# Kernel tuning notes

Hardware: AMD Instinct MI355X
Metric: run time of the kernel (lower is better)

Reference implementation:

```python
import jax, jax.numpy as jnp
import numpy as np

DEST = 64          # args['output_size']
NET = 256          # network_size = input_size - 3*dest_size
INPUT = NET + 3 * DEST  # 448
B, N = 4, 2048


def setup_inputs() -> dict:
    key = jax.random.key(0)
    ks = jax.random.split(key, 9)
    node_feature = jax.random.normal(ks[0], (B, N, INPUT), jnp.float32)
    adj_forward = jax.random.uniform(ks[1], (B, N, N), jnp.float32)
    adj_backward = jax.random.uniform(ks[2], (B, N, N), jnp.float32)
    s = 1.0 / np.sqrt(2 * DEST)
    Wf = jax.random.normal(ks[3], (2 * DEST, DEST), jnp.float32) * s
    bf = jnp.zeros((DEST,), jnp.float32)
    Wb = jax.random.normal(ks[4], (2 * DEST, DEST), jnp.float32) * s
    bb = jnp.zeros((DEST,), jnp.float32)
    W_emb = jax.random.normal(ks[5], (NET, 2 * DEST), jnp.float32) / np.sqrt(NET)
    b_emb = jnp.zeros((2 * DEST,), jnp.float32)
    return {"node_feature": node_feature, "adj_forward": adj_forward,
            "adj_backward": adj_backward, "Wf": Wf, "bf": bf,
            "Wb": Wb, "bb": bb, "W_emb": W_emb, "b_emb": b_emb}


def _gcn(x, adj, W, b):
    # GCN layer: aggregate neighbors then project. x: [B,N,2d], adj: [B,N,N]
    h = jnp.einsum('bmn,bnf->bmf', adj, x)  # message passing
    return h @ W + b                         # [B,N,d]


def reference(node_feature, adj_forward, adj_backward, Wf, bf, Wb, bb, W_emb, b_emb):
    dyn = node_feature[:, :, :DEST]                 # [B,N,d]
    struct = node_feature[:, :, DEST:3 * DEST]      # [B,N,2d]
    stat = node_feature[:, :, 3 * DEST:]            # [B,N,NET]
    fwd_code = dyn * _gcn(struct, adj_forward, Wf, bf)
    bwd_code = dyn * _gcn(struct, adj_backward, Wb, bb)
    emb = jnp.concatenate((fwd_code, bwd_code), axis=2)  # [B,N,2d]
    gate = jax.nn.sigmoid(stat @ W_emb + b_emb)           # [B,N,2d]
    return emb * gate
```

## Files before the change

kernel.cpp:

```cpp
#include <hip/hip_runtime.h>
#include <hip/hip_bf16.h>
#include <math.h>

#define BB    4
#define NNODE 2048
#define DST   64
#define NETW  256
#define INPT  448

typedef float f32x4 __attribute__((ext_vector_type(4)));
typedef short s16x8 __attribute__((ext_vector_type(8)));

#define MFMA(a, b, c) __builtin_amdgcn_mfma_f32_16x16x32_bf16((a), (b), (c), 0, 0, 0)

__device__ __align__(16) unsigned short g_WcatT[128 * 128];
__device__ __align__(16) unsigned short g_WembT[128 * 256];
__device__ __align__(16) unsigned short g_Ut[BB * 128 * NNODE];
__device__ __align__(16) float          g_G2[BB * NNODE * 128];

__device__ __forceinline__ unsigned bf16pk(float a, float b) {
    unsigned ua = __builtin_bit_cast(unsigned, a);
    unsigned ub = __builtin_bit_cast(unsigned, b);
    ua += 0x7fffu + ((ua >> 16) & 1u);
    ub += 0x7fffu + ((ub >> 16) & 1u);
    return (ua >> 16) | (ub & 0xffff0000u);
}
__device__ __forceinline__ unsigned short bf16b(float a) {
    unsigned ua = __builtin_bit_cast(unsigned, a);
    ua += 0x7fffu + ((ua >> 16) & 1u);
    return (unsigned short)(ua >> 16);
}
__device__ __forceinline__ s16x8 pack8(float4 x, float4 y) {
    union { unsigned u[4]; s16x8 s; } r;
    r.u[0] = bf16pk(x.x, x.y);
    r.u[1] = bf16pk(x.z, x.w);
    r.u[2] = bf16pk(y.x, y.y);
    r.u[3] = bf16pk(y.z, y.w);
    return r.s;
}

__global__ void k_weights(const float* __restrict__ Wf, const float* __restrict__ Wb,
                          const float* __restrict__ We) {
    int t = blockIdx.x * blockDim.x + threadIdx.x;
    int stride = gridDim.x * blockDim.x;
    for (int i = t; i < 128 * 128; i += stride) {
        int j = i >> 7, f = i & 127;
        float v = (j < 64) ? Wf[f * 64 + j] : Wb[f * 64 + (j - 64)];
        g_WcatT[i] = bf16b(v);
    }
    for (int i = t; i < 128 * 256; i += stride) {
        int c = i >> 8, k = i & 255;
        g_WembT[i] = bf16b(We[k * 128 + c]);
    }
}

__global__ __launch_bounds__(256) void k_prep(const float* __restrict__ nfeat,
                                              const float* __restrict__ bemb) {
    int w  = threadIdx.x >> 6;
    int l  = threadIdx.x & 63;
    int lr = l & 15, lc = l >> 4;
    int bid = blockIdx.x;

    if (bid < 512) {
        int b = bid >> 7;
        int nbase = (bid & 127) * 16;
        f32x4 acc[2] = {};
        #pragma unroll
        for (int kg = 0; kg < 4; ++kg) {
            s16x8 a0 = *(const s16x8*)&g_WcatT[((2 * w + 0) * 16 + lr) * 128 + kg * 32 + lc * 8];
            s16x8 a1 = *(const s16x8*)&g_WcatT[((2 * w + 1) * 16 + lr) * 128 + kg * 32 + lc * 8];
            const float* p = nfeat + (size_t)(b * NNODE + nbase + lr) * INPT + DST + kg * 32 + lc * 8;
            float4 x0 = *(const float4*)p;
            float4 x1 = *(const float4*)(p + 4);
            s16x8 bfr = pack8(x0, x1);
            acc[0] = MFMA(a0, bfr, acc[0]);
            acc[1] = MFMA(a1, bfr, acc[1]);
        }
        #pragma unroll
        for (int ja = 0; ja < 2; ++ja)
            #pragma unroll
            for (int r = 0; r < 4; ++r) {
                int j = (2 * w + ja) * 16 + lc * 4 + r;
                g_Ut[(size_t)(b * 128 + j) * NNODE + nbase + lr] = bf16b(acc[ja][r]);
            }
    } else {
        int bid2 = bid - 512;
        int b = bid2 >> 7;
        int mbase = (bid2 & 127) * 16;
        f32x4 acc[2] = {};
        #pragma unroll
        for (int kg = 0; kg < 8; ++kg) {
            const float* p = nfeat + (size_t)(b * NNODE + mbase + lr) * INPT + 3 * DST + kg * 32 + lc * 8;
            float4 x0 = *(const float4*)p;
            float4 x1 = *(const float4*)(p + 4);
            s16x8 a = pack8(x0, x1);
            #pragma unroll
            for (int ca = 0; ca < 2; ++ca) {
                int nf = 2 * w + ca;
                s16x8 bfr = *(const s16x8*)&g_WembT[(nf * 16 + lr) * 256 + kg * 32 + lc * 8];
                acc[ca] = MFMA(a, bfr, acc[ca]);
            }
        }
        #pragma unroll
        for (int ca = 0; ca < 2; ++ca) {
            int c = (2 * w + ca) * 16 + lr;
            float be = bemb[c];
            #pragma unroll
            for (int r = 0; r < 4; ++r) {
                int mm = mbase + lc * 4 + r;
                float v = acc[ca][r] + be;
                float g = 1.0f / (1.0f + expf(-v));
                g_G2[(size_t)(b * NNODE + mm) * 128 + c] =
                    g * nfeat[(size_t)(b * NNODE + mm) * INPT + (c & 63)];
            }
        }
    }
}

#define KW 8
__global__ __launch_bounds__(512) void k_main(const float* __restrict__ adjf,
                                              const float* __restrict__ adjb,
                                              const float* __restrict__ biasf,
                                              const float* __restrict__ biasb,
                                              float* __restrict__ out) {
    int bid  = blockIdx.x;
    int tile = bid & 127;
    int dir  = (bid >> 7) & 1;
    int b    = bid >> 8;
    int w  = threadIdx.x >> 6;
    int l  = threadIdx.x & 63;
    int lr = l & 15, lc = l >> 4;

    const float* adj  = dir ? adjb : adjf;
    const float* bias = dir ? biasb : biasf;
    int m0 = tile * 16;
    int k0 = w * 256;
    const float* arow = adj + (size_t)(b * NNODE + m0 + lr) * NNODE + k0 + lc * 8;
    const unsigned short* ut = g_Ut + (size_t)(b * 128 + dir * 64) * NNODE + k0;

    f32x4 acc[4] = {};
    #pragma unroll
    for (int ki = 0; ki < 8; ++ki) {
        const float4* pa = (const float4*)(arow + ki * 32);
        float4 x0 = pa[0];
        float4 x1 = pa[1];
        s16x8 a = pack8(x0, x1);
        #pragma unroll
        for (int nf = 0; nf < 4; ++nf) {
            s16x8 bfr = *(const s16x8*)&ut[(nf * 16 + lr) * NNODE + ki * 32 + lc * 8];
            acc[nf] = MFMA(a, bfr, acc[nf]);
        }
    }

    __shared__ float lds[KW][16][64];
    #pragma unroll
    for (int nf = 0; nf < 4; ++nf)
        #pragma unroll
        for (int r = 0; r < 4; ++r)
            lds[w][nf * 4 + r][l] = acc[nf][r];
    __syncthreads();

    if (w < 4) {
        #pragma unroll
        for (int r = 0; r < 4; ++r) {
            float s = 0.f;
            #pragma unroll
            for (int wp = 0; wp < KW; ++wp)
                s += lds[wp][w * 4 + r][l];
            int col = w * 16 + lr;
            int m   = m0 + lc * 4 + r;
            size_t o = (size_t)(b * NNODE + m) * 128 + dir * 64 + col;
            out[o] = (s + bias[col]) * g_G2[o];
        }
    }
}

extern "C" void kernel_launch(void* const* d_in, const int* in_sizes, int n_in,
                              void* d_out, int out_size, void* d_ws, size_t ws_size,
                              hipStream_t stream) {
    (void)in_sizes; (void)n_in; (void)d_ws; (void)ws_size; (void)out_size;
    const float* nfeat = (const float*)d_in[0];
    const float* adjf  = (const float*)d_in[1];
    const float* adjb  = (const float*)d_in[2];
    const float* Wf    = (const float*)d_in[3];
    const float* bf    = (const float*)d_in[4];
    const float* Wb    = (const float*)d_in[5];
    const float* bb    = (const float*)d_in[6];
    const float* We    = (const float*)d_in[7];
    const float* bemb  = (const float*)d_in[8];
    float* out = (float*)d_out;

    hipLaunchKernelGGL(k_weights, dim3(64),   dim3(256), 0, stream, Wf, Wb, We);
    hipLaunchKernelGGL(k_prep,    dim3(1024), dim3(256), 0, stream, nfeat, bemb);
    hipLaunchKernelGGL(k_main,    dim3(1024), dim3(512), 0, stream, adjf, adjb, bf, bb, out);
}
```

Measured before the change: 224.1 us.

## Pre-swizzle MFMA fragments, stage adjacency through LDS with coalesced loads and prefetch

```diff
diff --git a/kernel.cpp b/kernel.cpp
--- a/kernel.cpp
+++ b/kernel.cpp
@@ -2,174 +2,240 @@
 #include <hip/hip_bf16.h>
 #include <math.h>
 
-#define BB    4
-#define NNODE 2048
-#define DST   64
-#define NETW  256
-#define INPT  448
+#define BB   4
+#define NN   2048
+#define INPT 448
 
 typedef float f32x4 __attribute__((ext_vector_type(4)));
 typedef short s16x8 __attribute__((ext_vector_type(8)));
-
-#define MFMA(a, b, c) __builtin_amdgcn_mfma_f32_16x16x32_bf16((a), (b), (c), 0, 0, 0)
-
-__device__ __align__(16) unsigned short g_WcatT[128 * 128];
-__device__ __align__(16) unsigned short g_WembT[128 * 256];
-__device__ __align__(16) unsigned short g_Ut[BB * 128 * NNODE];
-__device__ __align__(16) float          g_G2[BB * NNODE * 128];
-
-__device__ __forceinline__ unsigned bf16pk(float a, float b) {
-    unsigned ua = __builtin_bit_cast(unsigned, a);
-    unsigned ub = __builtin_bit_cast(unsigned, b);
+typedef unsigned int u32;
+
+#define MFMA(a,b,c) __builtin_amdgcn_mfma_f32_16x16x32_bf16((a),(b),(c),0,0,0)
+
+__device__ __align__(16) unsigned short g_WcatF[4*8*64*8];
+__device__ __align__(16) unsigned short g_WembF[8*8*64*8];
+__device__ __align__(16) unsigned short g_UtF[BB*2*64*4*64*8];
+__device__ __align__(16) float          g_G2[BB*NN*128];
+
+__device__ __forceinline__ u32 bf16pk(float a, float b) {
+    u32 ua = __builtin_bit_cast(u32, a);
+    u32 ub = __builtin_bit_cast(u32, b);
     ua += 0x7fffu + ((ua >> 16) & 1u);
     ub += 0x7fffu + ((ub >> 16) & 1u);
     return (ua >> 16) | (ub & 0xffff0000u);
 }
 __device__ __forceinline__ unsigned short bf16b(float a) {
-    unsigned ua = __builtin_bit_cast(unsigned, a);
+    u32 ua = __builtin_bit_cast(u32, a);
     ua += 0x7fffu + ((ua >> 16) & 1u);
     return (unsigned short)(ua >> 16);
 }
-__device__ __forceinline__ s16x8 pack8(float4 x, float4 y) {
-    union { unsigned u[4]; s16x8 s; } r;
-    r.u[0] = bf16pk(x.x, x.y);
-    r.u[1] = bf16pk(x.z, x.w);
-    r.u[2] = bf16pk(y.x, y.y);
-    r.u[3] = bf16pk(y.z, y.w);
-    return r.s;
-}
 
 __global__ void k_weights(const float* __restrict__ Wf, const float* __restrict__ Wb,
                           const float* __restrict__ We) {
-    int t = blockIdx.x * blockDim.x + threadIdx.x;
-    int stride = gridDim.x * blockDim.x;
-    for (int i = t; i < 128 * 128; i += stride) {
-        int j = i >> 7, f = i & 127;
-        float v = (j < 64) ? Wf[f * 64 + j] : Wb[f * 64 + (j - 64)];
-        g_WcatT[i] = bf16b(v);
-    }
-    for (int i = t; i < 128 * 256; i += stride) {
-        int c = i >> 8, k = i & 255;
-        g_WembT[i] = bf16b(We[k * 128 + c]);
+    int t = blockIdx.x * 256 + threadIdx.x;
+    if (t < 2048) {
+        int l = t & 63, jf = (t >> 6) & 7, kg = t >> 9;
+        int j  = jf * 16 + (l & 15);
+        int f0 = kg * 32 + (l >> 4) * 8;
+        union { u32 u[4]; s16x8 s; } r;
+        #pragma unroll
+        for (int e = 0; e < 8; e += 2) {
+            float v0 = (j < 64) ? Wf[(f0 + e    ) * 64 + j] : Wb[(f0 + e    ) * 64 + (j - 64)];
+            float v1 = (j < 64) ? Wf[(f0 + e + 1) * 64 + j] : Wb[(f0 + e + 1) * 64 + (j - 64)];
+            r.u[e >> 1] = bf16pk(v0, v1);
+        }
+        *(s16x8*)&g_WcatF[t * 8] = r.s;
+    } else if (t < 2048 + 4096) {
+        int idx = t - 2048;
+        int l = idx & 63, cf = (idx >> 6) & 7, kg = idx >> 9;
+        int c  = cf * 16 + (l & 15);
+        int k0 = kg * 32 + (l >> 4) * 8;
+        union { u32 u[4]; s16x8 s; } r;
+        #pragma unroll
+        for (int e = 0; e < 8; e += 2)
+            r.u[e >> 1] = bf16pk(We[(k0 + e) * 128 + c], We[(k0 + e + 1) * 128 + c]);
+        *(s16x8*)&g_WembF[idx * 8] = r.s;
     }
 }
 
 __global__ __launch_bounds__(256) void k_prep(const float* __restrict__ nfeat,
                                               const float* __restrict__ bemb) {
-    int w  = threadIdx.x >> 6;
-    int l  = threadIdx.x & 63;
-    int lr = l & 15, lc = l >> 4;
+    __shared__ __align__(16) char sm[24576];
+    int tid = threadIdx.x;
+    int w = tid >> 6, l = tid & 63, lr = l & 15, lc = l >> 4;
     int bid = blockIdx.x;
 
-    if (bid < 512) {
-        int b = bid >> 7;
-        int nbase = (bid & 127) * 16;
-        f32x4 acc[2] = {};
+    if (bid < 256) {
+        int b = bid >> 6, nb = bid & 63;
+        unsigned short* ss = (unsigned short*)sm;
+        unsigned short* ob = (unsigned short*)(sm + 8192);
+        const float* base = nfeat + (size_t)(b * NN + nb * 32) * INPT;
+        #pragma unroll
+        for (int i = 0; i < 4; ++i) {
+            int node = w * 8 + i * 2 + (l >> 5);
+            int c4 = (l & 31) * 4;
+            float4 v = *(const float4*)(base + (size_t)node * INPT + 64 + c4);
+            int off = node * 256 + c4 * 2; off ^= (node & 7) << 4;
+            uint2 pk; pk.x = bf16pk(v.x, v.y); pk.y = bf16pk(v.z, v.w);
+            *(uint2*)((char*)ss + off) = pk;
+        }
+        __syncthreads();
+        f32x4 acc[2][2] = {};
         #pragma unroll
         for (int kg = 0; kg < 4; ++kg) {
-            s16x8 a0 = *(const s16x8*)&g_WcatT[((2 * w + 0) * 16 + lr) * 128 + kg * 32 + lc * 8];
-            s16x8 a1 = *(const s16x8*)&g_WcatT[((2 * w + 1) * 16 + lr) * 128 + kg * 32 + lc * 8];
-            const float* p = nfeat + (size_t)(b * NNODE + nbase + lr) * INPT + DST + kg * 32 + lc * 8;
-            float4 x0 = *(const float4*)p;
-            float4 x1 = *(const float4*)(p + 4);
-            s16x8 bfr = pack8(x0, x1);
-            acc[0] = MFMA(a0, bfr, acc[0]);
-            acc[1] = MFMA(a1, bfr, acc[1]);
+            s16x8 a0 = *(const s16x8*)&g_WcatF[((kg * 8 + w * 2 + 0) * 64 + l) * 8];
+            s16x8 a1 = *(const s16x8*)&g_WcatF[((kg * 8 + w * 2 + 1) * 64 + l) * 8];
+            #pragma unroll
+            for (int na = 0; na < 2; ++na) {
+                int off = (na * 16 + lr) * 256 + kg * 64 + lc * 16; off ^= (lr & 7) << 4;
+                s16x8 bf = *(const s16x8*)((char*)ss + off);
+                acc[0][na] = MFMA(a0, bf, acc[0][na]);
+                acc[1][na] = MFMA(a1, bf, acc[1][na]);
+            }
         }
         #pragma unroll
         for (int ja = 0; ja < 2; ++ja)
             #pragma unroll
-            for (int r = 0; r < 4; ++r) {
-                int j = (2 * w + ja) * 16 + lc * 4 + r;
-                g_Ut[(size_t)(b * 128 + j) * NNODE + nbase + lr] = bf16b(acc[ja][r]);
-            }
+            for (int na = 0; na < 2; ++na)
+                #pragma unroll
+                for (int r = 0; r < 4; ++r) {
+                    int j = w * 32 + ja * 16 + lc * 4 + r;
+                    int n = na * 16 + lr;
+                    ob[j * 32 + n] = bf16b(acc[ja][na][r]);
+                }
+        __syncthreads();
+        #pragma unroll
+        for (int q = 0; q < 2; ++q) {
+            int idx = q * 256 + tid;
+            int dirx = idx >> 8, nf = (idx >> 6) & 3, ll = idx & 63;
+            int j = dirx * 64 + nf * 16 + (ll & 15);
+            int n0 = (ll >> 4) * 8;
+            s16x8 v = *(const s16x8*)&ob[j * 32 + n0];
+            *(s16x8*)&g_UtF[((((size_t)(b * 2 + dirx) * 64 + nb) * 4 + nf) * 64 + ll) * 8] = v;
+        }
     } else {
-        int bid2 = bid - 512;
-        int b = bid2 >> 7;
-        int mbase = (bid2 & 127) * 16;
-        f32x4 acc[2] = {};
+        int bid2 = bid - 256;
+        int b = bid2 >> 6, mb = bid2 & 63;
+        unsigned short* ss = (unsigned short*)sm;
+        float* dyls = (float*)(sm + 16384);
+        const float* base = nfeat + (size_t)(b * NN + mb * 32) * INPT;
+        #pragma unroll
+        for (int i = 0; i < 8; ++i) {
+            int row = w * 8 + i;
+            float4 v = *(const float4*)(base + (size_t)row * INPT + 192 + l * 4);
+            int off = row * 512 + l * 8; off ^= (row & 7) << 4;
+            uint2 pk; pk.x = bf16pk(v.x, v.y); pk.y = bf16pk(v.z, v.w);
+            *(uint2*)((char*)ss + off) = pk;
+        }
+        #pragma unroll
+        for (int i = 0; i < 2; ++i) {
+            int row = w * 8 + i * 4 + lc;
+            float4 v = *(const float4*)(base + (size_t)row * INPT + lr * 4);
+            *(float4*)&dyls[row * 64 + lr * 4] = v;
+        }
+        __syncthreads();
+        f32x4 acc[2][2] = {};
         #pragma unroll
         for (int kg = 0; kg < 8; ++kg) {
-            const float* p = nfeat + (size_t)(b * NNODE + mbase + lr) * INPT + 3 * DST + kg * 32 + lc * 8;
-            float4 x0 = *(const float4*)p;
-            float4 x1 = *(const float4*)(p + 4);
-            s16x8 a = pack8(x0, x1);
-            #pragma unroll
-            for (int ca = 0; ca < 2; ++ca) {
-                int nf = 2 * w + ca;
-                s16x8 bfr = *(const s16x8*)&g_WembT[(nf * 16 + lr) * 256 + kg * 32 + lc * 8];
-                acc[ca] = MFMA(a, bfr, acc[ca]);
-            }
-        }
-        #pragma unroll
-        for (int ca = 0; ca < 2; ++ca) {
-            int c = (2 * w + ca) * 16 + lr;
+            s16x8 a0, a1;
+            {
+                int off = lr * 512 + kg * 64 + lc * 16; off ^= (lr & 7) << 4;
+                a0 = *(const s16x8*)((char*)ss + off);
+                a1 = *(const s16x8*)((char*)ss + off + 8192);
+            }
+            #pragma unroll
+            for (int cfi = 0; cfi < 2; ++cfi) {
+                s16x8 bf = *(const s16x8*)&g_WembF[((kg * 8 + w * 2 + cfi) * 64 + l) * 8];
+                acc[cfi][0] = MFMA(a0, bf, acc[cfi][0]);
+                acc[cfi][1] = MFMA(a1, bf, acc[cfi][1]);
+            }
+        }
+        #pragma unroll
+        for (int cfi = 0; cfi < 2; ++cfi) {
+            int c = (w * 2 + cfi) * 16 + lr;
             float be = bemb[c];
             #pragma unroll
-            for (int r = 0; r < 4; ++r) {
-                int mm = mbase + lc * 4 + r;
-                float v = acc[ca][r] + be;
-                float g = 1.0f / (1.0f + expf(-v));
-                g_G2[(size_t)(b * NNODE + mm) * 128 + c] =
-                    g * nfeat[(size_t)(b * NNODE + mm) * INPT + (c & 63)];
-            }
-        }
-    }
-}
-
-#define KW 8
-__global__ __launch_bounds__(512) void k_main(const float* __restrict__ adjf,
-                                              const float* __restrict__ adjb,
-                                              const float* __restrict__ biasf,
-                                              const float* __restrict__ biasb,
-                                              float* __restrict__ out) {
-    int bid  = blockIdx.x;
-    int tile = bid & 127;
-    int dir  = (bid >> 7) & 1;
-    int b    = bid >> 8;
-    int w  = threadIdx.x >> 6;
-    int l  = threadIdx.x & 63;
-    int lr = l & 15, lc = l >> 4;
-
+            for (int mf = 0; mf < 2; ++mf)
+                #pragma unroll
+                for (int r = 0; r < 4; ++r) {
+                    int m = mf * 16 + lc * 4 + r;
+                    float v = acc[cfi][mf][r] + be;
+                    float g = 1.0f / (1.0f + expf(-v));
+                    g_G2[(size_t)(b * NN + mb * 32 + m) * 128 + c] = g * dyls[m * 64 + (c & 63)];
+                }
+        }
+    }
+}
+
+__global__ __launch_bounds__(512, 4) void k_main(const float* __restrict__ adjf,
+                                                 const float* __restrict__ adjb,
+                                                 const float* __restrict__ biasf,
+                                                 const float* __restrict__ biasb,
+                                                 float* __restrict__ out) {
+    __shared__ __align__(16) char sm[32768];
+    int tid = threadIdx.x;
+    int w = tid >> 6, l = tid & 63, lr = l & 15, lc = l >> 4;
+    int bid = blockIdx.x;
+    int tile = bid & 127, dir = (bid >> 7) & 1, b = bid >> 8;
     const float* adj  = dir ? adjb : adjf;
     const float* bias = dir ? biasb : biasf;
     int m0 = tile * 16;
-    int k0 = w * 256;
-    const float* arow = adj + (size_t)(b * NNODE + m0 + lr) * NNODE + k0 + lc * 8;
-    const unsigned short* ut = g_Ut + (size_t)(b * 128 + dir * 64) * NNODE + k0;
+    const unsigned short* utF = g_UtF + (size_t)(b * 2 + dir) * 131072;
+    const float* ag = adj + (size_t)(b * NN + m0) * NN + w * 256;
+    char* abase = sm + w * 4096;
 
     f32x4 acc[4] = {};
+    float4 av[4];
     #pragma unroll
-    for (int ki = 0; ki < 8; ++ki) {
-        const float4* pa = (const float4*)(arow + ki * 32);
-        float4 x0 = pa[0];
-        float4 x1 = pa[1];
-        s16x8 a = pack8(x0, x1);
-        #pragma unroll
-        for (int nf = 0; nf < 4; ++nf) {
-            s16x8 bfr = *(const s16x8*)&ut[(nf * 16 + lr) * NNODE + ki * 32 + lc * 8];
-            acc[nf] = MFMA(a, bfr, acc[nf]);
-        }
-    }
-
-    __shared__ float lds[KW][16][64];
+    for (int i = 0; i < 4; ++i)
+        av[i] = *(const float4*)(ag + (size_t)(4 * i + lc) * NN + (l & 15) * 4);
+
+    for (int c = 0; c < 4; ++c) {
+        float4 avn[4];
+        if (c < 3) {
+            #pragma unroll
+            for (int i = 0; i < 4; ++i)
+                avn[i] = *(const float4*)(ag + (size_t)(4 * i + lc) * NN + (c + 1) * 64 + (l & 15) * 4);
+        }
+        char* abuf = abase + (c & 1) * 2048;
+        #pragma unroll
+        for (int i = 0; i < 4; ++i) {
+            int row = 4 * i + lc;
+            int off = row * 128 + (l & 15) * 8; off ^= (row & 7) << 4;
+            uint2 pk; pk.x = bf16pk(av[i].x, av[i].y); pk.y = bf16pk(av[i].z, av[i].w);
+            *(uint2*)(abuf + off) = pk;
+        }
+        #pragma unroll
+        for (int ii = 0; ii < 2; ++ii) {
+            int off = lr * 128 + ii * 64 + lc * 16; off ^= (lr & 7) << 4;
+            s16x8 af = *(const s16x8*)(abuf + off);
+            int kk = w * 8 + c * 2 + ii;
+            #pragma unroll
+            for (int nf = 0; nf < 4; ++nf) {
+                s16x8 bf = *(const s16x8*)&utF[((kk * 4 + nf) * 64 + l) * 8];
+                acc[nf] = MFMA(af, bf, acc[nf]);
+            }
+        }
+        if (c < 3) { av[0] = avn[0]; av[1] = avn[1]; av[2] = avn[2]; av[3] = avn[3]; }
+    }
+
+    float* red = (float*)sm;
     #pragma unroll
     for (int nf = 0; nf < 4; ++nf)
         #pragma unroll
         for (int r = 0; r < 4; ++r)
-            lds[w][nf * 4 + r][l] = acc[nf][r];
+            red[(w * 16 + nf * 4 + r) * 64 + l] = acc[nf][r];
     __syncthreads();
-
     if (w < 4) {
         #pragma unroll
         for (int r = 0; r < 4; ++r) {
             float s = 0.f;
             #pragma unroll
-            for (int wp = 0; wp < KW; ++wp)
-                s += lds[wp][w * 4 + r][l];
+            for (int wp = 0; wp < 8; ++wp)
+                s += red[(wp * 16 + w * 4 + r) * 64 + l];
             int col = w * 16 + lr;
-            int m   = m0 + lc * 4 + r;
-            size_t o = (size_t)(b * NNODE + m) * 128 + dir * 64 + col;
+            int m = m0 + lc * 4 + r;
+            size_t o = (size_t)(b * NN + m) * 128 + dir * 64 + col;
             out[o] = (s + bias[col]) * g_G2[o];
         }
     }
@@ -190,7 +256,7 @@
     const float* bemb  = (const float*)d_in[8];
     float* out = (float*)d_out;
 
-    hipLaunchKernelGGL(k_weights, dim3(64),   dim3(256), 0, stream, Wf, Wb, We);
-    hipLaunchKernelGGL(k_prep,    dim3(1024), dim3(256), 0, stream, nfeat, bemb);
+    hipLaunchKernelGGL(k_weights, dim3(24),   dim3(256), 0, stream, Wf, Wb, We);
+    hipLaunchKernelGGL(k_prep,    dim3(512),  dim3(256), 0, stream, nfeat, bemb);
     hipLaunchKernelGGL(k_main,    dim3(1024), dim3(512), 0, stream, adjf, adjb, bf, bb, out);
 }
```

Result: faster. 187.3 us (-16.4%).
